# Performance work log

Hardware: AMD Instinct MI355X
Metric: run time of the kernel (lower is better)

## Reference

```python
import jax, jax.numpy as jnp
import numpy as np

N = 4096

def setup_inputs() -> dict:
    key = jax.random.key(0)
    k1, k2, k3 = jax.random.split(key, 3)
    x = jax.random.normal(k1, (N, N), dtype=jnp.float32)
    # nn.Linear(N, N, bias=False) weight matrices, shape [out, in] = [N, N]
    s = 1.0 / np.sqrt(N)
    W_r = jax.random.uniform(k2, (N, N), dtype=jnp.float32, minval=-s, maxval=s)
    W_i = jax.random.uniform(k3, (N, N), dtype=jnp.float32, minval=-s, maxval=s)
    return {"x": x, "W_r": W_r, "W_i": W_i}

def reference(x, W_r, W_i):
    # Row pass: fft_in_rows[i] = Linear_real(x[i]) + 1j * Linear_imag(x[i])
    #   => R = x @ W_r^T + 1j * (x @ W_i^T)
    R_r = x @ W_r.T            # [N, N]
    R_i = x @ W_i.T            # [N, N]
    # Column pass: fft_in_cols[:, i] = fft_in_rows[:, i] @ (W_r + 1j W_i)
    #   => C = W^T @ R with W = W_r + 1j W_i (complex matmul in real arithmetic)
    C_r = W_r.T @ R_r - W_i.T @ R_i
    C_i = W_r.T @ R_i + W_i.T @ R_r
    # res = cat([real, imag], dim=1) -> [N, 2N]
    return jnp.concatenate([C_r, C_i], axis=1)
```

## Files before the change

### kernel.cpp

```cpp
#include <hip/hip_runtime.h>
#include <hip/hip_bf16.h>

#define NN 4096

typedef unsigned short u16;
using bf16x8 = __attribute__((ext_vector_type(8))) short;
using f32x4  = __attribute__((ext_vector_type(4))) float;

__device__ inline u16 f2bf(float f) {
    union { float f; unsigned u; } c; c.f = f;
    unsigned r = (c.u + 0x7fffu + ((c.u >> 16) & 1u)) >> 16;
    return (u16)r;
}
__device__ inline float bf2f(u16 b) {
    union { unsigned u; float f; } c; c.u = ((unsigned)b) << 16;
    return c.f;
}

__device__ inline void gld16(const void* g, void* l) {
    __builtin_amdgcn_global_load_lds(
        (const __attribute__((address_space(1))) void*)g,
        (__attribute__((address_space(3))) void*)l, 16, 0, 0);
}

__global__ __launch_bounds__(256) void cvt_bf16(const float* __restrict__ s,
                                                u16* __restrict__ d) {
    size_t i = ((size_t)blockIdx.x * 256 + threadIdx.x) * 8;
    float4 v0 = *(const float4*)(s + i);
    float4 v1 = *(const float4*)(s + i + 4);
    bf16x8 o;
    o[0] = (short)f2bf(v0.x); o[1] = (short)f2bf(v0.y);
    o[2] = (short)f2bf(v0.z); o[3] = (short)f2bf(v0.w);
    o[4] = (short)f2bf(v1.x); o[5] = (short)f2bf(v1.y);
    o[6] = (short)f2bf(v1.z); o[7] = (short)f2bf(v1.w);
    *(bf16x8*)(d + i) = o;
}

__global__ __launch_bounds__(256) void wprep(const float* __restrict__ Wr,
                                             const float* __restrict__ Wi,
                                             u16* __restrict__ WrT,
                                             u16* __restrict__ WiT,
                                             u16* __restrict__ SA) {
    __shared__ float tr[32][33], ti[32][33];
    int x  = blockIdx.x * 32 + threadIdx.x;
    int y0 = blockIdx.y * 32;
#pragma unroll
    for (int j = 0; j < 32; j += 8) {
        tr[threadIdx.y + j][threadIdx.x] = Wr[(size_t)(y0 + threadIdx.y + j) * NN + x];
        ti[threadIdx.y + j][threadIdx.x] = Wi[(size_t)(y0 + threadIdx.y + j) * NN + x];
    }
    __syncthreads();
    int x2 = blockIdx.y * 32 + threadIdx.x;
    int y2 = blockIdx.x * 32;
#pragma unroll
    for (int j = 0; j < 32; j += 8) {
        float a = tr[threadIdx.x][threadIdx.y + j];
        float b = ti[threadIdx.x][threadIdx.y + j];
        size_t o = (size_t)(y2 + threadIdx.y + j) * NN + x2;
        WrT[o] = f2bf(a);
        WiT[o] = f2bf(b);
        SA[o]  = f2bf(a + b);
    }
}

__global__ __launch_bounds__(256) void presum(const u16* __restrict__ a,
                                              const u16* __restrict__ b,
                                              u16* __restrict__ d) {
    size_t i = ((size_t)blockIdx.x * 256 + threadIdx.x) * 8;
    bf16x8 va = *(const bf16x8*)(a + i);
    bf16x8 vb = *(const bf16x8*)(b + i);
    bf16x8 o;
#pragma unroll
    for (int j = 0; j < 8; j++)
        o[j] = (short)f2bf(bf2f((u16)va[j]) + bf2f((u16)vb[j]));
    *(bf16x8*)(d + i) = o;
}

__global__ __launch_bounds__(256) void combine(float* __restrict__ out,
                                               const float* __restrict__ M2) {
    size_t i = ((size_t)blockIdx.x * 256 + threadIdx.x) * 4;
    size_t m = i >> 12, n = i & 4095;
    float4 v1 = *(float4*)(out + m * 8192 + n);
    float4 v3 = *(float4*)(out + m * 8192 + 4096 + n);
    float4 v2 = *(const float4*)(M2 + m * 4096 + n);
    float4 cr, ci;
    cr.x = v1.x - v2.x; ci.x = v3.x - v1.x - v2.x;
    cr.y = v1.y - v2.y; ci.y = v3.y - v1.y - v2.y;
    cr.z = v1.z - v2.z; ci.z = v3.z - v1.z - v2.z;
    cr.w = v1.w - v2.w; ci.w = v3.w - v1.w - v2.w;
    *(float4*)(out + m * 8192 + n) = cr;
    *(float4*)(out + m * 8192 + 4096 + n) = ci;
}

#define P_BAR  __builtin_amdgcn_s_barrier()
#define P_SCH  __builtin_amdgcn_sched_barrier(0)
#define P_LGKM do { asm volatile("s_waitcnt lgkmcnt(0)" ::: "memory"); \
                    __builtin_amdgcn_sched_barrier(0); } while (0)
#define VMW(N) do { asm volatile("s_waitcnt vmcnt(" #N ")" ::: "memory"); \
                    __builtin_amdgcn_sched_barrier(0); } while (0)

#define SGA(NB, KN) do { \
    gld16(A + aoff0 + (KN), &sm2[NB][0][tid * 8]); \
    gld16(A + aoff1 + (KN), &sm2[NB][0][4096 + tid * 8]); \
} while (0)
#define SGB(NB, KN) do { \
    gld16(Bp + boff0 + (KN), &sm2[NB][1][tid * 8]); \
    gld16(Bp + boff1 + (KN), &sm2[NB][1][4096 + tid * 8]); \
} while (0)

#define K256(CB, NB, KN, DOSTG, V) do { \
    bf16x8 a[4], b[4], c[4]; \
    VMW(V); P_BAR; P_SCH; \
    _Pragma("unroll") \
    for (int i_ = 0; i_ < 4; i_++) \
        a[i_] = *(const bf16x8*)&sm2[CB][0][(wr128 + i_ * 16 + rl) * 32 + kg]; \
    _Pragma("unroll") \
    for (int j_ = 0; j_ < 4; j_++) \
        b[j_] = *(const bf16x8*)&sm2[CB][1][(wc64 + j_ * 16 + rl) * 32 + kg]; \
    if (DOSTG) SGA(NB, KN); \
    P_LGKM; \
    __builtin_amdgcn_s_setprio(1); \
    _Pragma("unroll") \
    for (int i_ = 0; i_ < 4; i_++) \
        _Pragma("unroll") \
        for (int j_ = 0; j_ < 4; j_++) \
            acc[i_][j_] = __builtin_amdgcn_mfma_f32_16x16x32_bf16(a[i_], b[j_], acc[i_][j_], 0, 0, 0); \
    __builtin_amdgcn_s_setprio(0); \
    _Pragma("unroll") \
    for (int i_ = 0; i_ < 4; i_++) \
        c[i_] = *(const bf16x8*)&sm2[CB][0][(wr128 + 64 + i_ * 16 + rl) * 32 + kg]; \
    if (DOSTG) SGB(NB, KN); \
    P_LGKM; \
    __builtin_amdgcn_s_setprio(1); \
    _Pragma("unroll") \
    for (int i_ = 0; i_ < 4; i_++) \
        _Pragma("unroll") \
        for (int j_ = 0; j_ < 4; j_++) \
            acc[4 + i_][j_] = __builtin_amdgcn_mfma_f32_16x16x32_bf16(c[i_], b[j_], acc[4 + i_][j_], 0, 0, 0); \
    __builtin_amdgcn_s_setprio(0); \
} while (0)

template <int OM>
__global__ __launch_bounds__(512, 2) void gemm256k(
    const u16* __restrict__ A, const u16* __restrict__ Bp,
    u16* __restrict__ Cb, float* __restrict__ Cf, int cs) {
    __shared__ u16 sm2[4][2][8192];

    const int brow = blockIdx.y * 256;
    const int bcol = blockIdx.x * 256;

    const int tid  = threadIdx.x;
    const int lane = tid & 63;
    const int wid  = tid >> 6;
    const int wr128 = (wid >> 2) * 128;
    const int wc64  = (wid & 3) * 64;
    const int rl = lane & 15;
    const int kq = lane >> 4;
    const int kg = (kq ^ ((rl >> 1) & 3)) * 8;

    const int r0 = tid >> 2;
    const int lb = (tid & 3) ^ ((r0 >> 1) & 3);
    const size_t aoff0 = (size_t)(brow + r0) * NN + lb * 8;
    const size_t aoff1 = aoff0 + (size_t)128 * NN;
    const size_t boff0 = (size_t)(bcol + r0) * NN + lb * 8;
    const size_t boff1 = boff0 + (size_t)128 * NN;

    f32x4 acc[8][4] = {};

    SGA(0, 0); SGB(0, 0); SGA(1, 32); SGB(1, 32);

    for (int tb = 0; tb < 31; ++tb) {
        const size_t k0 = (size_t)tb * 128;
        K256(0, 2, k0 + 64,  1, 4);
        K256(1, 3, k0 + 96,  1, 4);
        K256(2, 0, k0 + 128, 1, 4);
        K256(3, 1, k0 + 160, 1, 4);
    }
    K256(0, 2, 4032, 1, 4);
    K256(1, 3, 4064, 1, 4);
    K256(2, 0, 0,    0, 4);
    K256(3, 0, 0,    0, 0);

    const int rg = kq * 4;
#pragma unroll
    for (int fr = 0; fr < 8; fr++)
#pragma unroll
        for (int fc = 0; fc < 4; fc++) {
            const int col = bcol + wc64 + fc * 16 + rl;
#pragma unroll
            for (int e = 0; e < 4; e++) {
                const int row = brow + wr128 + fr * 16 + rg + e;
                if (OM == 0)
                    Cb[(size_t)row * NN + col] = f2bf(acc[fr][fc][e]);
                else
                    Cf[(size_t)row * cs + col] = acc[fr][fc][e];
            }
        }
}

extern "C" void kernel_launch(void* const* d_in, const int* in_sizes, int n_in,
                              void* d_out, int out_size, void* d_ws, size_t ws_size,
                              hipStream_t stream) {
    const float* x  = (const float*)d_in[0];
    const float* Wr = (const float*)d_in[1];
    const float* Wi = (const float*)d_in[2];
    float* out = (float*)d_out;

    const size_t SZ = (size_t)NN * NN;
    u16* ws = (u16*)d_ws;
    u16* s0 = ws;
    u16* s1 = ws + SZ;
    u16* s2 = ws + 2 * SZ;
    u16* s3 = ws + 3 * SZ;
    u16* s4 = ws + 4 * SZ;
    u16* s5 = ws + 5 * SZ;
    float* M2 = (float*)s2;

    cvt_bf16<<<8192, 256, 0, stream>>>(x,  s0);
    cvt_bf16<<<8192, 256, 0, stream>>>(Wr, s1);
    cvt_bf16<<<8192, 256, 0, stream>>>(Wi, s2);

    gemm256k<0><<<dim3(16, 16), 512, 0, stream>>>(s1, s0, s3, nullptr, 0);
    gemm256k<0><<<dim3(16, 16), 512, 0, stream>>>(s2, s0, s4, nullptr, 0);

    wprep<<<dim3(128, 128), dim3(32, 8), 0, stream>>>(Wr, Wi, s0, s1, s2);
    presum<<<8192, 256, 0, stream>>>(s3, s4, s5);

    gemm256k<1><<<dim3(16, 16), 512, 0, stream>>>(s2, s5, nullptr, out + NN, 2 * NN);
    gemm256k<1><<<dim3(16, 16), 512, 0, stream>>>(s0, s3, nullptr, out,      2 * NN);
    gemm256k<1><<<dim3(16, 16), 512, 0, stream>>>(s1, s4, nullptr, M2,       NN);

    combine<<<16384, 256, 0, stream>>>(out, M2);
}
```

Before: 740.1 us.

## Deepen GEMM LDS prefetch to three stages and double-buffer register fragments

```diff
diff --git a/kernel.cpp b/kernel.cpp
--- a/kernel.cpp
+++ b/kernel.cpp
@@ -96,6 +96,8 @@
 #define P_SCH  __builtin_amdgcn_sched_barrier(0)
 #define P_LGKM do { asm volatile("s_waitcnt lgkmcnt(0)" ::: "memory"); \
                     __builtin_amdgcn_sched_barrier(0); } while (0)
+#define LGKM4  do { asm volatile("s_waitcnt lgkmcnt(4)" ::: "memory"); \
+                    __builtin_amdgcn_sched_barrier(0); } while (0)
 #define VMW(N) do { asm volatile("s_waitcnt vmcnt(" #N ")" ::: "memory"); \
                     __builtin_amdgcn_sched_barrier(0); } while (0)
 
@@ -108,36 +110,35 @@
     gld16(Bp + boff1 + (KN), &sm2[NB][1][4096 + tid * 8]); \
 } while (0)
 
-#define K256(CB, NB, KN, DOSTG, V) do { \
-    bf16x8 a[4], b[4], c[4]; \
-    VMW(V); P_BAR; P_SCH; \
-    _Pragma("unroll") \
-    for (int i_ = 0; i_ < 4; i_++) \
-        a[i_] = *(const bf16x8*)&sm2[CB][0][(wr128 + i_ * 16 + rl) * 32 + kg]; \
-    _Pragma("unroll") \
-    for (int j_ = 0; j_ < 4; j_++) \
-        b[j_] = *(const bf16x8*)&sm2[CB][1][(wc64 + j_ * 16 + rl) * 32 + kg]; \
-    if (DOSTG) SGA(NB, KN); \
-    P_LGKM; \
+#define CL16(AF, BF, OFF) do { \
     __builtin_amdgcn_s_setprio(1); \
     _Pragma("unroll") \
     for (int i_ = 0; i_ < 4; i_++) \
         _Pragma("unroll") \
         for (int j_ = 0; j_ < 4; j_++) \
-            acc[i_][j_] = __builtin_amdgcn_mfma_f32_16x16x32_bf16(a[i_], b[j_], acc[i_][j_], 0, 0, 0); \
+            acc[(OFF) + i_][j_] = __builtin_amdgcn_mfma_f32_16x16x32_bf16(AF[i_], BF[j_], acc[(OFF) + i_][j_], 0, 0, 0); \
     __builtin_amdgcn_s_setprio(0); \
+} while (0)
+
+#define STEP(AC, BC, AN, BN_, CBUF, NBUF, SBUF, KS, DOSTG, VWTOK, RDNEXT) do { \
+    bf16x8 cfr[4]; \
     _Pragma("unroll") \
     for (int i_ = 0; i_ < 4; i_++) \
-        c[i_] = *(const bf16x8*)&sm2[CB][0][(wr128 + 64 + i_ * 16 + rl) * 32 + kg]; \
-    if (DOSTG) SGB(NB, KN); \
+        cfr[i_] = *(const bf16x8*)&sm2[CBUF][0][(wr128 + 64 + i_ * 16 + rl) * 32 + kg]; \
+    if (DOSTG) { SGA(SBUF, KS); SGB(SBUF, KS); } \
+    LGKM4; \
+    CL16(AC, BC, 0); \
     P_LGKM; \
-    __builtin_amdgcn_s_setprio(1); \
-    _Pragma("unroll") \
-    for (int i_ = 0; i_ < 4; i_++) \
+    CL16(cfr, BC, 4); \
+    VWTOK; P_BAR; P_SCH; \
+    if (RDNEXT) { \
         _Pragma("unroll") \
-        for (int j_ = 0; j_ < 4; j_++) \
-            acc[4 + i_][j_] = __builtin_amdgcn_mfma_f32_16x16x32_bf16(c[i_], b[j_], acc[4 + i_][j_], 0, 0, 0); \
-    __builtin_amdgcn_s_setprio(0); \
+        for (int i_ = 0; i_ < 4; i_++) { \
+            AN[i_]  = *(const bf16x8*)&sm2[NBUF][0][(wr128 + i_ * 16 + rl) * 32 + kg]; \
+            BN_[i_] = *(const bf16x8*)&sm2[NBUF][1][(wc64  + i_ * 16 + rl) * 32 + kg]; \
+        } \
+        P_SCH; \
+    } \
 } while (0)
 
 template <int OM>
@@ -166,20 +167,30 @@
     const size_t boff1 = boff0 + (size_t)128 * NN;
 
     f32x4 acc[8][4] = {};
-
-    SGA(0, 0); SGB(0, 0); SGA(1, 32); SGB(1, 32);
+    bf16x8 aX[4], bX[4], aY[4], bY[4];
+
+    SGA(0, 0);  SGB(0, 0);
+    SGA(1, 32); SGB(1, 32);
+    SGA(2, 64); SGB(2, 64);
+    VMW(8); P_BAR; P_SCH;
+#pragma unroll
+    for (int i_ = 0; i_ < 4; i_++) {
+        aX[i_] = *(const bf16x8*)&sm2[0][0][(wr128 + i_ * 16 + rl) * 32 + kg];
+        bX[i_] = *(const bf16x8*)&sm2[0][1][(wc64  + i_ * 16 + rl) * 32 + kg];
+    }
+    P_SCH;
 
     for (int tb = 0; tb < 31; ++tb) {
-        const size_t k0 = (size_t)tb * 128;
-        K256(0, 2, k0 + 64,  1, 4);
-        K256(1, 3, k0 + 96,  1, 4);
-        K256(2, 0, k0 + 128, 1, 4);
-        K256(3, 1, k0 + 160, 1, 4);
-    }
-    K256(0, 2, 4032, 1, 4);
-    K256(1, 3, 4064, 1, 4);
-    K256(2, 0, 0,    0, 4);
-    K256(3, 0, 0,    0, 0);
+        const size_t k3 = ((size_t)tb * 4 + 3) * 32;
+        STEP(aX, bX, aY, bY, 0, 1, 3, k3,       1, VMW(8), 1);
+        STEP(aY, bY, aX, bX, 1, 2, 0, k3 + 32,  1, VMW(8), 1);
+        STEP(aX, bX, aY, bY, 2, 3, 1, k3 + 64,  1, VMW(8), 1);
+        STEP(aY, bY, aX, bX, 3, 0, 2, k3 + 96,  1, VMW(8), 1);
+    }
+    STEP(aX, bX, aY, bY, 0, 1, 3, (size_t)127 * 32, 1, VMW(8), 1);
+    STEP(aY, bY, aX, bX, 1, 2, 0, 0, 0, VMW(4), 1);
+    STEP(aX, bX, aY, bY, 2, 3, 0, 0, 0, VMW(0), 1);
+    STEP(aY, bY, aX, bX, 3, 0, 0, 0, 0, ((void)0), 0);
 
     const int rg = kq * 4;
 #pragma unroll
```

Measured after the change: 905.2 us. 22.3% more time.

## Restructure GEMM mainloop into 64-wide K tiles with eight-phase A/B staging

Applied to the files above, without the earlier changes.

```diff
diff --git a/kernel.cpp b/kernel.cpp
--- a/kernel.cpp
+++ b/kernel.cpp
@@ -93,58 +93,61 @@
 }
 
 #define P_BAR  __builtin_amdgcn_s_barrier()
-#define P_SCH  __builtin_amdgcn_sched_barrier(0)
 #define P_LGKM do { asm volatile("s_waitcnt lgkmcnt(0)" ::: "memory"); \
                     __builtin_amdgcn_sched_barrier(0); } while (0)
 #define VMW(N) do { asm volatile("s_waitcnt vmcnt(" #N ")" ::: "memory"); \
                     __builtin_amdgcn_sched_barrier(0); } while (0)
 
-#define SGA(NB, KN) do { \
-    gld16(A + aoff0 + (KN), &sm2[NB][0][tid * 8]); \
-    gld16(A + aoff1 + (KN), &sm2[NB][0][4096 + tid * 8]); \
+#define MF(a_, b_, c_) __builtin_amdgcn_mfma_f32_16x16x32_bf16(a_, b_, c_, 0, 0, 0)
+
+#define RDA(c, fr, k32) (*(const bf16x8*)&sA[c][wm][((fr)*16 + rl)*64 + ((((k32)*4 + kq) ^ rl7))*8])
+#define RDB(c, fc, k32) (*(const bf16x8*)&sB[c][bh][(bro + (fc)*16 + rl)*64 + ((((k32)*4 + kq) ^ rl7))*8])
+
+#define BLOADALL(c) do { \
+    b00 = RDB(c,0,0); b01 = RDB(c,0,1); b10 = RDB(c,1,0); b11 = RDB(c,1,1); \
+    b20 = RDB(c,2,0); b21 = RDB(c,2,1); b30 = RDB(c,3,0); b31 = RDB(c,3,1); } while (0)
+
+#define STG_A(c, H, KT) do { \
+    gld16(A + aoff + (size_t)((H)*128)*NN + (KT),    &sA[c][H][tid*8]); \
+    gld16(A + aoff + (size_t)((H)*128+64)*NN + (KT), &sA[c][H][4096 + tid*8]); } while (0)
+#define STG_B(c, H, KT) do { \
+    gld16(Bp + boff + (size_t)((H)*128)*NN + (KT),    &sB[c][H][tid*8]); \
+    gld16(Bp + boff + (size_t)((H)*128+64)*NN + (KT), &sB[c][H][4096 + tid*8]); } while (0)
+
+#define PHASE(c, p, BLOAD, STG, GATE) do { \
+    bf16x8 a0 = RDA(c, 2*(p), 0),   a1 = RDA(c, 2*(p), 1); \
+    bf16x8 a2 = RDA(c, 2*(p)+1, 0), a3 = RDA(c, 2*(p)+1, 1); \
+    BLOAD; \
+    STG; \
+    P_BAR; P_LGKM; \
+    __builtin_amdgcn_s_setprio(1); \
+    acc[2*(p)][0]   = MF(a0, b00, acc[2*(p)][0]); \
+    acc[2*(p)][1]   = MF(a0, b10, acc[2*(p)][1]); \
+    acc[2*(p)][2]   = MF(a0, b20, acc[2*(p)][2]); \
+    acc[2*(p)][3]   = MF(a0, b30, acc[2*(p)][3]); \
+    acc[2*(p)+1][0] = MF(a2, b00, acc[2*(p)+1][0]); \
+    acc[2*(p)+1][1] = MF(a2, b10, acc[2*(p)+1][1]); \
+    acc[2*(p)+1][2] = MF(a2, b20, acc[2*(p)+1][2]); \
+    acc[2*(p)+1][3] = MF(a2, b30, acc[2*(p)+1][3]); \
+    acc[2*(p)][0]   = MF(a1, b01, acc[2*(p)][0]); \
+    acc[2*(p)][1]   = MF(a1, b11, acc[2*(p)][1]); \
+    acc[2*(p)][2]   = MF(a1, b21, acc[2*(p)][2]); \
+    acc[2*(p)][3]   = MF(a1, b31, acc[2*(p)][3]); \
+    acc[2*(p)+1][0] = MF(a3, b01, acc[2*(p)+1][0]); \
+    acc[2*(p)+1][1] = MF(a3, b11, acc[2*(p)+1][1]); \
+    acc[2*(p)+1][2] = MF(a3, b21, acc[2*(p)+1][2]); \
+    acc[2*(p)+1][3] = MF(a3, b31, acc[2*(p)+1][3]); \
+    __builtin_amdgcn_s_setprio(0); \
+    GATE; \
+    P_BAR; \
 } while (0)
-#define SGB(NB, KN) do { \
-    gld16(Bp + boff0 + (KN), &sm2[NB][1][tid * 8]); \
-    gld16(Bp + boff1 + (KN), &sm2[NB][1][4096 + tid * 8]); \
-} while (0)
-
-#define K256(CB, NB, KN, DOSTG, V) do { \
-    bf16x8 a[4], b[4], c[4]; \
-    VMW(V); P_BAR; P_SCH; \
-    _Pragma("unroll") \
-    for (int i_ = 0; i_ < 4; i_++) \
-        a[i_] = *(const bf16x8*)&sm2[CB][0][(wr128 + i_ * 16 + rl) * 32 + kg]; \
-    _Pragma("unroll") \
-    for (int j_ = 0; j_ < 4; j_++) \
-        b[j_] = *(const bf16x8*)&sm2[CB][1][(wc64 + j_ * 16 + rl) * 32 + kg]; \
-    if (DOSTG) SGA(NB, KN); \
-    P_LGKM; \
-    __builtin_amdgcn_s_setprio(1); \
-    _Pragma("unroll") \
-    for (int i_ = 0; i_ < 4; i_++) \
-        _Pragma("unroll") \
-        for (int j_ = 0; j_ < 4; j_++) \
-            acc[i_][j_] = __builtin_amdgcn_mfma_f32_16x16x32_bf16(a[i_], b[j_], acc[i_][j_], 0, 0, 0); \
-    __builtin_amdgcn_s_setprio(0); \
-    _Pragma("unroll") \
-    for (int i_ = 0; i_ < 4; i_++) \
-        c[i_] = *(const bf16x8*)&sm2[CB][0][(wr128 + 64 + i_ * 16 + rl) * 32 + kg]; \
-    if (DOSTG) SGB(NB, KN); \
-    P_LGKM; \
-    __builtin_amdgcn_s_setprio(1); \
-    _Pragma("unroll") \
-    for (int i_ = 0; i_ < 4; i_++) \
-        _Pragma("unroll") \
-        for (int j_ = 0; j_ < 4; j_++) \
-            acc[4 + i_][j_] = __builtin_amdgcn_mfma_f32_16x16x32_bf16(c[i_], b[j_], acc[4 + i_][j_], 0, 0, 0); \
-    __builtin_amdgcn_s_setprio(0); \
-} while (0)
 
 template <int OM>
-__global__ __launch_bounds__(512, 2) void gemm256k(
+__global__ __launch_bounds__(512, 2) void gemm256p(
     const u16* __restrict__ A, const u16* __restrict__ Bp,
     u16* __restrict__ Cb, float* __restrict__ Cf, int cs) {
-    __shared__ u16 sm2[4][2][8192];
+    __shared__ u16 sA[2][2][8192];
+    __shared__ u16 sB[2][2][8192];
 
     const int brow = blockIdx.y * 256;
     const int bcol = blockIdx.x * 256;
@@ -152,35 +155,49 @@
     const int tid  = threadIdx.x;
     const int lane = tid & 63;
     const int wid  = tid >> 6;
-    const int wr128 = (wid >> 2) * 128;
-    const int wc64  = (wid & 3) * 64;
-    const int rl = lane & 15;
-    const int kq = lane >> 4;
-    const int kg = (kq ^ ((rl >> 1) & 3)) * 8;
-
-    const int r0 = tid >> 2;
-    const int lb = (tid & 3) ^ ((r0 >> 1) & 3);
-    const size_t aoff0 = (size_t)(brow + r0) * NN + lb * 8;
-    const size_t aoff1 = aoff0 + (size_t)128 * NN;
-    const size_t boff0 = (size_t)(bcol + r0) * NN + lb * 8;
-    const size_t boff1 = boff0 + (size_t)128 * NN;
+    const int wm   = wid >> 2;
+    const int wn   = wid & 3;
+    const int bh   = wn >> 1;
+    const int bro  = (wn & 1) * 64;
+    const int rl   = lane & 15;
+    const int kq   = lane >> 4;
+    const int rl7  = rl & 7;
+
+    const int sr = tid >> 3;
+    const int lb = (tid & 7) ^ (sr & 7);
+    const size_t aoff = (size_t)(brow + sr) * NN + lb * 8;
+    const size_t boff = (size_t)(bcol + sr) * NN + lb * 8;
 
     f32x4 acc[8][4] = {};
-
-    SGA(0, 0); SGB(0, 0); SGA(1, 32); SGB(1, 32);
-
-    for (int tb = 0; tb < 31; ++tb) {
-        const size_t k0 = (size_t)tb * 128;
-        K256(0, 2, k0 + 64,  1, 4);
-        K256(1, 3, k0 + 96,  1, 4);
-        K256(2, 0, k0 + 128, 1, 4);
-        K256(3, 1, k0 + 160, 1, 4);
+    bf16x8 b00, b01, b10, b11, b20, b21, b30, b31;
+
+    STG_A(0, 0, 0);  STG_A(0, 1, 0);
+    STG_B(0, 0, 0);  STG_B(0, 1, 0);
+    STG_B(1, 0, 64); STG_B(1, 1, 64);
+    VMW(4); P_BAR;
+
+    for (int i = 0; i < 31; ++i) {
+        const size_t k1 = ((size_t)2 * i + 1) * 64;
+        const size_t k2 = k1 + 64, k3 = k2 + 64;
+        PHASE(0, 0, BLOADALL(0), STG_A(1, 0, k1), ((void)0));
+        PHASE(0, 1, ((void)0),   STG_A(1, 1, k1), ((void)0));
+        PHASE(0, 2, ((void)0),   STG_B(0, 0, k2), ((void)0));
+        PHASE(0, 3, ((void)0),   STG_B(0, 1, k2), VMW(4));
+        PHASE(1, 0, BLOADALL(1), STG_A(0, 0, k2), ((void)0));
+        PHASE(1, 1, ((void)0),   STG_A(0, 1, k2), ((void)0));
+        PHASE(1, 2, ((void)0),   STG_B(1, 0, k3), ((void)0));
+        PHASE(1, 3, ((void)0),   STG_B(1, 1, k3), VMW(4));
     }
-    K256(0, 2, 4032, 1, 4);
-    K256(1, 3, 4064, 1, 4);
-    K256(2, 0, 0,    0, 4);
-    K256(3, 0, 0,    0, 0);
-
+    PHASE(0, 0, BLOADALL(0), STG_A(1, 0, 4032), ((void)0));
+    PHASE(0, 1, ((void)0),   STG_A(1, 1, 4032), ((void)0));
+    PHASE(0, 2, ((void)0),   ((void)0),         ((void)0));
+    PHASE(0, 3, ((void)0),   ((void)0),         VMW(0));
+    PHASE(1, 0, BLOADALL(1), ((void)0),         ((void)0));
+    PHASE(1, 1, ((void)0),   ((void)0),         ((void)0));
+    PHASE(1, 2, ((void)0),   ((void)0),         ((void)0));
+    PHASE(1, 3, ((void)0),   ((void)0),         ((void)0));
+
+    const int wr128 = wm * 128, wc64 = wn * 64;
     const int rg = kq * 4;
 #pragma unroll
     for (int fr = 0; fr < 8; fr++)
@@ -220,15 +237,15 @@
     cvt_bf16<<<8192, 256, 0, stream>>>(Wr, s1);
     cvt_bf16<<<8192, 256, 0, stream>>>(Wi, s2);
 
-    gemm256k<0><<<dim3(16, 16), 512, 0, stream>>>(s1, s0, s3, nullptr, 0);
-    gemm256k<0><<<dim3(16, 16), 512, 0, stream>>>(s2, s0, s4, nullptr, 0);
+    gemm256p<0><<<dim3(16, 16), 512, 0, stream>>>(s1, s0, s3, nullptr, 0);
+    gemm256p<0><<<dim3(16, 16), 512, 0, stream>>>(s2, s0, s4, nullptr, 0);
 
     wprep<<<dim3(128, 128), dim3(32, 8), 0, stream>>>(Wr, Wi, s0, s1, s2);
     presum<<<8192, 256, 0, stream>>>(s3, s4, s5);
 
-    gemm256k<1><<<dim3(16, 16), 512, 0, stream>>>(s2, s5, nullptr, out + NN, 2 * NN);
-    gemm256k<1><<<dim3(16, 16), 512, 0, stream>>>(s0, s3, nullptr, out,      2 * NN);
-    gemm256k<1><<<dim3(16, 16), 512, 0, stream>>>(s1, s4, nullptr, M2,       NN);
+    gemm256p<1><<<dim3(16, 16), 512, 0, stream>>>(s2, s5, nullptr, out + NN, 2 * NN);
+    gemm256p<1><<<dim3(16, 16), 512, 0, stream>>>(s0, s3, nullptr, out,      2 * NN);
+    gemm256p<1><<<dim3(16, 16), 512, 0, stream>>>(s1, s4, nullptr, M2,       NN);
 
     combine<<<16384, 256, 0, stream>>>(out, M2);
 }
```

Result: slower. 794.8 us (+7.4%).
